# Optimization experiments

Measured on AMD Instinct MI355X. Metric: run time of the kernel, lower is better.

## Reference

```python
import jax, jax.numpy as jnp
import numpy as np

CHANNEL = 1
ALPHA = 1.0
EPS = 1e-10
SHAPE = (1, CHANNEL, 160, 192, 160)


def _sobel_kernels(channel):
    s2 = np.array([[-1., 0., 1.], [-2., 0., 2.], [-1., 0., 1.]], dtype=np.float32)
    # sobel.repeat(channel,1,3,1,1): 2D kernel tiled along depth -> k[d,h,w] = s2[h,w]
    kx = np.tile(s2[None, :, :], (3, 1, 1))
    ky = np.tile(s2.T[None, :, :], (3, 1, 1))
    kz = np.array([[[-1., -1., -1.], [-2., -2., -2.], [-1., -1., -1.]],
                   [[0., 0., 0.], [0., 0., 0.], [0., 0., 0.]],
                   [[1., 1., 1.], [2., 2., 2.], [1., 1., 1.]]], dtype=np.float32)
    def rep(k):  # -> [channel, 1, 3, 3, 3] for depthwise conv
        return jnp.asarray(np.tile(k[None, None], (channel, 1, 1, 1, 1)))
    return rep(kx), rep(ky), rep(kz)


def _conv3d(x, k, channel):
    # torch F.conv3d (cross-correlation), padding=1, groups=channel
    return jax.lax.conv_general_dilated(
        x, k, window_strides=(1, 1, 1), padding=((1, 1), (1, 1), (1, 1)),
        dimension_numbers=('NCDHW', 'OIDHW', 'NCDHW'),
        feature_group_count=channel)


def setup_inputs() -> dict:
    key = jax.random.key(0)
    k1, k2, k3 = jax.random.split(key, 3)
    M = jax.random.normal(k1, SHAPE, dtype=jnp.float32)
    S = jax.random.normal(k2, SHAPE, dtype=jnp.float32)
    flow = jax.random.normal(k3, (SHAPE[0], 3) + SHAPE[2:], dtype=jnp.float32)
    return {"M": M, "S": S, "flow": flow}


def reference(M, S, flow):
    kx, ky, kz = _sobel_kernels(CHANNEL)
    Idiff = M - S
    Sx = _conv3d(S, kx, CHANNEL)
    Sy = _conv3d(S, ky, CHANNEL)
    Sz = _conv3d(S, kz, CHANNEL)
    Mx = _conv3d(M, kx, CHANNEL)
    My = _conv3d(M, ky, CHANNEL)
    Mz = _conv3d(M, kz, CHANNEL)
    Sxyz_mag = Sx ** 2 + Sy ** 2 + Sz ** 2
    Mxyz_mag = Mx ** 2 + My ** 2 + Mz ** 2
    denom_S = Sxyz_mag + (ALPHA ** 2) * Idiff ** 2 + 1e-10
    denom_M = Mxyz_mag + (ALPHA ** 2) * Idiff ** 2 + 1e-10
    Ux = Idiff * (Sx / denom_S + Mx / denom_M)
    Uy = Idiff * (Sy / denom_S + My / denom_M)
    Uz = Idiff * (Sz / denom_S + Mz / denom_M)
    demons_ori_xz = jnp.arctan(Ux / (Uz + EPS))
    demons_ori_yz = jnp.arctan(Uy / (Uz + EPS))
    flow_ori_xz = jnp.arctan(flow[:, 0] / (flow[:, 2] + EPS))
    flow_ori_yz = jnp.arctan(flow[:, 1] / (flow[:, 2] + EPS))
    ori_error = jnp.mean((flow_ori_xz - demons_ori_xz) ** 2) + \
                jnp.mean((flow_ori_yz - demons_ori_yz) ** 2)
    return ori_error
```

## Files before the change

### kernel.cpp

```cpp
#include <hip/hip_runtime.h>
#include <math.h>

#define DD 160
#define HH 192
#define WW 160
#define TW 32
#define THB 16
#define TD 8
#define HW (HH * WW)
#define NVOX (DD * HW)
#define HTW 34
#define HTH 18
#define LSTR 34
#define HALO (HTH * HTW)

typedef float v2f __attribute__((ext_vector_type(2)));

__device__ __forceinline__ v2f vrcp(v2f a) {
    v2f r;
    r.x = __builtin_amdgcn_rcpf(a.x);
    r.y = __builtin_amdgcn_rcpf(a.y);
    return r;
}

__device__ __forceinline__ v2f atan_ratio(v2f num, v2f den) {
    v2f a = __builtin_elementwise_abs(num);
    v2f b = __builtin_elementwise_abs(den);
    v2f mn = __builtin_elementwise_min(a, b);
    v2f mx = __builtin_elementwise_max(a, b);
    v2f x = mn * vrcp(mx);
    v2f x2 = x * x;
    v2f p = __builtin_elementwise_fma(x2,
            __builtin_elementwise_fma(x2,
            __builtin_elementwise_fma(x2,
            __builtin_elementwise_fma(x2,
            __builtin_elementwise_fma(x2, (v2f)(-0.0117212f), (v2f)(0.05265332f)),
            (v2f)(-0.11643287f)), (v2f)(0.19354346f)), (v2f)(-0.33262347f)),
            (v2f)(0.99997726f));
    p *= x;
    v2f q = 1.57079632679489662f - p;
    v2f res;
    res.x = a.x > b.x ? q.x : p.x;
    res.y = a.y > b.y ? q.y : p.y;
    unsigned sx = (__float_as_uint(num.x) ^ __float_as_uint(den.x)) & 0x80000000u;
    unsigned sy = (__float_as_uint(num.y) ^ __float_as_uint(den.y)) & 0x80000000u;
    res.x = __uint_as_float(__float_as_uint(res.x) | sx);
    res.y = __uint_as_float(__float_as_uint(res.y) | sy);
    return res;
}

__global__ __launch_bounds__(256) void demons_ori_kernel(
    const float* __restrict__ Mv, const float* __restrict__ Sv,
    const float* __restrict__ flow, float* __restrict__ out)
{
    __shared__ float buf[2][2][HTH * LSTR];
    __shared__ float redbuf[4];

    const int tid = threadIdx.x;
    const int lane = tid & 63;
    const int wid = tid >> 6;
    const int i16 = lane & 15;
    const int r   = wid * 4 + (lane >> 4);
    const int tw2 = 2 * i16;
    const int w0 = blockIdx.x * TW;
    const int h0 = blockIdx.y * THB;
    const int d0 = blockIdx.z * TD;

    const bool has2 = (tid < HALO - 512);
    int gb0, gb1, gb2 = 0;
    bool ok0, ok1, ok2 = false;
    {
        int i = tid;
        int hh = i / HTW, ww = i - HTW * hh;
        int gh = h0 + hh - 1, gw = w0 + ww - 1;
        ok0 = (gh >= 0 && gh < HH && gw >= 0 && gw < WW);
        gb0 = gh * WW + gw;
        i = tid + 256;
        hh = i / HTW; ww = i - HTW * hh;
        gh = h0 + hh - 1; gw = w0 + ww - 1;
        ok1 = (gh >= 0 && gh < HH && gw >= 0 && gw < WW);
        gb1 = gh * WW + gw;
        if (has2) {
            i = tid + 512;
            hh = i / HTW; ww = i - HTW * hh;
            gh = h0 + hh - 1; gw = w0 + ww - 1;
            ok2 = (gh >= 0 && gh < HH && gw >= 0 && gw < WW);
            gb2 = gh * WW + gw;
        }
    }

    float pS0 = 0.f, pM0 = 0.f, pS1 = 0.f, pM1 = 0.f, pS2 = 0.f, pM2 = 0.f;

    auto issue = [&](int d) {
        const bool din = (d >= 0) && (d < DD);
        const size_t base = (size_t)d * HW;
        pS0 = (din && ok0) ? Sv[base + gb0] : 0.f;
        pM0 = (din && ok0) ? Mv[base + gb0] : 0.f;
        pS1 = (din && ok1) ? Sv[base + gb1] : 0.f;
        pM1 = (din && ok1) ? Mv[base + gb1] : 0.f;
        pS2 = (din && ok2) ? Sv[base + gb2] : 0.f;
        pM2 = (din && ok2) ? Mv[base + gb2] : 0.f;
    };
    auto commit = [&](int d) {
        float* __restrict__ bS = &buf[d & 1][0][0];
        float* __restrict__ bM = &buf[d & 1][1][0];
        bS[tid] = pS0;        bM[tid] = pM0;
        bS[tid + 256] = pS1;  bM[tid + 256] = pM1;
        if (has2) { bS[tid + 512] = pS2; bM[tid + 512] = pM2; }
    };

    const int rb = r * LSTR + tw2;
    auto fieldPartials = [&](const float* __restrict__ b,
                             v2f& Px, v2f& Py, v2f& Bq, v2f& Cq) {
        const float* p0 = b + rb;
        const float* p1 = p0 + LSTR;
        const float* p2 = p1 + LSTR;
        v2f lo0 = *(const v2f*)p0, hi0 = *(const v2f*)(p0 + 2);
        v2f lo1 = *(const v2f*)p1, hi1 = *(const v2f*)(p1 + 2);
        v2f lo2 = *(const v2f*)p2, hi2 = *(const v2f*)(p2 + 2);
        v2f X0 = hi0 - lo0, X1 = hi1 - lo1, X2 = hi2 - lo2;
        v2f m0 = (v2f){lo0.y, hi0.x};
        v2f m1 = (v2f){lo1.y, hi1.x};
        v2f m2 = (v2f){lo2.y, hi2.x};
        v2f s0 = lo0 + hi0, s1 = lo1 + hi1, s2 = lo2 + hi2;
        v2f W0 = __builtin_elementwise_fma(m0, (v2f)(2.f), s0);
        v2f W2 = __builtin_elementwise_fma(m2, (v2f)(2.f), s2);
        v2f I0 = s0 + m0, I1 = s1 + m1, I2 = s2 + m2;
        Px = __builtin_elementwise_fma(X1, (v2f)(2.f), X0) + X2;
        Py = W2 - W0;
        Bq = __builtin_elementwise_fma(I1, (v2f)(2.f), I0) + I2;
        Cq = m1;
    };

    v2f mSPx, mSPy, mSB, mSC, mMPx, mMPy, mMB, mMC;
    v2f zSPx, zSPy, zSB, zSC, zMPx, zMPy, zMB, zMC;
    v2f pSPx, pSPy, pSB, pSC, pMPx, pMPy, pMB, pMC;

    issue(d0 - 1);
    commit(d0 - 1);
    issue(d0);
    __syncthreads();
    fieldPartials(&buf[(d0 - 1) & 1][0][0], mSPx, mSPy, mSB, mSC);
    fieldPartials(&buf[(d0 - 1) & 1][1][0], mMPx, mMPy, mMB, mMC);
    commit(d0);
    issue(d0 + 1);
    __syncthreads();
    fieldPartials(&buf[d0 & 1][0][0], zSPx, zSPy, zSB, zSC);
    fieldPartials(&buf[d0 & 1][1][0], zMPx, zMPy, zMB, zMC);

    const size_t voffA = (size_t)(h0 + r) * WW + (w0 + tw2);
    v2f fFx, fFy, fFz;
    {
        size_t o = (size_t)d0 * HW + voffA;
        fFx = *(const v2f*)(flow + o);
        fFy = *(const v2f*)(flow + NVOX + o);
        fFz = *(const v2f*)(flow + 2 * (size_t)NVOX + o);
    }

    v2f vsum = (v2f){0.f, 0.f};

    #pragma unroll
    for (int dd = 0; dd < TD; ++dd) {
        const int d = d0 + dd;
        commit(d + 1);
        v2f nFx = (v2f){0.f, 0.f}, nFy = nFx, nFz = nFx;
        if (dd < TD - 1) {
            issue(d + 2);
            size_t o = (size_t)(d + 1) * HW + voffA;
            nFx = *(const v2f*)(flow + o);
            nFy = *(const v2f*)(flow + NVOX + o);
            nFz = *(const v2f*)(flow + 2 * (size_t)NVOX + o);
        }
        __syncthreads();
        fieldPartials(&buf[(d + 1) & 1][0][0], pSPx, pSPy, pSB, pSC);
        fieldPartials(&buf[(d + 1) & 1][1][0], pMPx, pMPy, pMB, pMC);

        v2f idf = zMC - zSC;
        v2f i2  = __builtin_elementwise_fma(idf, idf, (v2f)(1e-10f));
        v2f gxS = mSPx + zSPx + pSPx;
        v2f gyS = mSPy + zSPy + pSPy;
        v2f gzS = pSB - mSB;
        v2f gxM = mMPx + zMPx + pMPx;
        v2f gyM = mMPy + zMPy + pMPy;
        v2f gzM = pMB - mMB;
        v2f denS = __builtin_elementwise_fma(gxS, gxS,
                   __builtin_elementwise_fma(gyS, gyS,
                   __builtin_elementwise_fma(gzS, gzS, i2)));
        v2f denM = __builtin_elementwise_fma(gxM, gxM,
                   __builtin_elementwise_fma(gyM, gyM,
                   __builtin_elementwise_fma(gzM, gzM, i2)));
        v2f rS = vrcp(denS);
        v2f rM = vrcp(denM);
        v2f Ux = idf * __builtin_elementwise_fma(gxS, rS, gxM * rM);
        v2f Uy = idf * __builtin_elementwise_fma(gyS, rS, gyM * rM);
        v2f Uz = idf * __builtin_elementwise_fma(gzS, rS, gzM * rM);

        v2f uzp = Uz + 1e-10f;
        v2f dxz = atan_ratio(Ux, uzp);
        v2f dyz = atan_ratio(Uy, uzp);

        v2f fzp = fFz + 1e-10f;
        v2f fxz = atan_ratio(fFx, fzp);
        v2f fyz = atan_ratio(fFy, fzp);

        v2f e1 = fxz - dxz;
        v2f e2 = fyz - dyz;
        vsum = __builtin_elementwise_fma(e1, e1,
               __builtin_elementwise_fma(e2, e2, vsum));

        mSPx = zSPx; mSPy = zSPy; mSB = zSB; mSC = zSC;
        mMPx = zMPx; mMPy = zMPy; mMB = zMB; mMC = zMC;
        zSPx = pSPx; zSPy = pSPy; zSB = pSB; zSC = pSC;
        zMPx = pMPx; zMPy = pMPy; zMB = pMB; zMC = pMC;
        fFx = nFx; fFy = nFy; fFz = nFz;
    }

    float lsum = vsum.x + vsum.y;
    #pragma unroll
    for (int o = 32; o > 0; o >>= 1)
        lsum += __shfl_down(lsum, o, 64);
    if (lane == 0)
        redbuf[wid] = lsum;
    __syncthreads();
    if (tid == 0) {
        float s = redbuf[0] + redbuf[1] + redbuf[2] + redbuf[3];
        atomicAdd(out, s * (1.0f / (float)NVOX));
    }
}

extern "C" void kernel_launch(void* const* d_in, const int* in_sizes, int n_in,
                              void* d_out, int out_size, void* d_ws, size_t ws_size,
                              hipStream_t stream) {
    const float* Mv   = (const float*)d_in[0];
    const float* Sv   = (const float*)d_in[1];
    const float* flow = (const float*)d_in[2];
    float* out = (float*)d_out;

    hipMemsetAsync(out, 0, sizeof(float), stream);

    dim3 grid(WW / TW, HH / THB, DD / TD);
    demons_ori_kernel<<<grid, dim3(256), 0, stream>>>(Mv, Sv, flow, out);
}
```

Before: 129.5 us.

## Enlarge tile to 32x32 and compute four outputs per thread

The block tile height doubles from 16 to 32 rows, which shrinks the halo overhead per output voxel. Each thread now computes four adjacent outputs instead of two, reusing the shared LDS loads across both pairs and loading flow as float4. The cost is higher register pressure from keeping twice as many partials alive, five global loads per field per thread, and half as many blocks, which may reduce occupancy or latency hiding.

Measured after the change: 142.4 us. 1.1x slower.

```diff
diff --git a/kernel.cpp b/kernel.cpp
--- a/kernel.cpp
+++ b/kernel.cpp
@@ -5,16 +5,17 @@
 #define HH 192
 #define WW 160
 #define TW 32
-#define THB 16
+#define THB 32
 #define TD 8
 #define HW (HH * WW)
 #define NVOX (DD * HW)
 #define HTW 34
-#define HTH 18
+#define HTH 34
 #define LSTR 34
 #define HALO (HTH * HTW)
 
 typedef float v2f __attribute__((ext_vector_type(2)));
+typedef float v4f __attribute__((ext_vector_type(4)));
 
 __device__ __forceinline__ v2f vrcp(v2f a) {
     v2f r;
@@ -49,140 +50,109 @@
     return res;
 }
 
+struct Part { v2f Px, Py, B, C; };
+
 __global__ __launch_bounds__(256) void demons_ori_kernel(
     const float* __restrict__ Mv, const float* __restrict__ Sv,
     const float* __restrict__ flow, float* __restrict__ out)
 {
-    __shared__ float buf[2][2][HTH * LSTR];
+    __shared__ float buf[2][2][HALO];
     __shared__ float redbuf[4];
 
     const int tid = threadIdx.x;
     const int lane = tid & 63;
     const int wid = tid >> 6;
-    const int i16 = lane & 15;
-    const int r   = wid * 4 + (lane >> 4);
-    const int tw2 = 2 * i16;
+    const int r   = tid >> 3;
+    const int i8  = tid & 7;
+    const int tw4 = 4 * i8;
     const int w0 = blockIdx.x * TW;
     const int h0 = blockIdx.y * THB;
     const int d0 = blockIdx.z * TD;
 
-    const bool has2 = (tid < HALO - 512);
-    int gb0, gb1, gb2 = 0;
-    bool ok0, ok1, ok2 = false;
-    {
-        int i = tid;
+    const bool has4 = (tid < HALO - 1024);
+    int gb[5]; bool ok[5];
+    #pragma unroll
+    for (int s = 0; s < 5; ++s) {
+        int i = tid + 256 * s;
         int hh = i / HTW, ww = i - HTW * hh;
         int gh = h0 + hh - 1, gw = w0 + ww - 1;
-        ok0 = (gh >= 0 && gh < HH && gw >= 0 && gw < WW);
-        gb0 = gh * WW + gw;
-        i = tid + 256;
-        hh = i / HTW; ww = i - HTW * hh;
-        gh = h0 + hh - 1; gw = w0 + ww - 1;
-        ok1 = (gh >= 0 && gh < HH && gw >= 0 && gw < WW);
-        gb1 = gh * WW + gw;
-        if (has2) {
-            i = tid + 512;
-            hh = i / HTW; ww = i - HTW * hh;
-            gh = h0 + hh - 1; gw = w0 + ww - 1;
-            ok2 = (gh >= 0 && gh < HH && gw >= 0 && gw < WW);
-            gb2 = gh * WW + gw;
-        }
-    }
-
-    float pS0 = 0.f, pM0 = 0.f, pS1 = 0.f, pM1 = 0.f, pS2 = 0.f, pM2 = 0.f;
+        bool act = (s < 4) || has4;
+        ok[s] = act && (gh >= 0) && (gh < HH) && (gw >= 0) && (gw < WW);
+        gb[s] = gh * WW + gw;
+    }
+
+    float hS[5], hM[5];
 
     auto issue = [&](int d) {
-        const bool din = (d >= 0) && (d < DD);
+        const bool din = ((unsigned)d < (unsigned)DD);
         const size_t base = (size_t)d * HW;
-        pS0 = (din && ok0) ? Sv[base + gb0] : 0.f;
-        pM0 = (din && ok0) ? Mv[base + gb0] : 0.f;
-        pS1 = (din && ok1) ? Sv[base + gb1] : 0.f;
-        pM1 = (din && ok1) ? Mv[base + gb1] : 0.f;
-        pS2 = (din && ok2) ? Sv[base + gb2] : 0.f;
-        pM2 = (din && ok2) ? Mv[base + gb2] : 0.f;
+        #pragma unroll
+        for (int s = 0; s < 5; ++s) {
+            bool o = din && ok[s];
+            hS[s] = o ? Sv[base + gb[s]] : 0.f;
+            hM[s] = o ? Mv[base + gb[s]] : 0.f;
+        }
     };
     auto commit = [&](int d) {
         float* __restrict__ bS = &buf[d & 1][0][0];
         float* __restrict__ bM = &buf[d & 1][1][0];
-        bS[tid] = pS0;        bM[tid] = pM0;
-        bS[tid + 256] = pS1;  bM[tid + 256] = pM1;
-        if (has2) { bS[tid + 512] = pS2; bM[tid + 512] = pM2; }
-    };
-
-    const int rb = r * LSTR + tw2;
-    auto fieldPartials = [&](const float* __restrict__ b,
-                             v2f& Px, v2f& Py, v2f& Bq, v2f& Cq) {
+        #pragma unroll
+        for (int s = 0; s < 4; ++s) {
+            bS[tid + 256 * s] = hS[s];
+            bM[tid + 256 * s] = hM[s];
+        }
+        if (has4) { bS[tid + 1024] = hS[4]; bM[tid + 1024] = hM[4]; }
+    };
+
+    const int rb = r * LSTR + tw4;
+    auto fieldPartials = [&](const float* __restrict__ b, Part& A, Part& B) {
         const float* p0 = b + rb;
         const float* p1 = p0 + LSTR;
         const float* p2 = p1 + LSTR;
-        v2f lo0 = *(const v2f*)p0, hi0 = *(const v2f*)(p0 + 2);
-        v2f lo1 = *(const v2f*)p1, hi1 = *(const v2f*)(p1 + 2);
-        v2f lo2 = *(const v2f*)p2, hi2 = *(const v2f*)(p2 + 2);
-        v2f X0 = hi0 - lo0, X1 = hi1 - lo1, X2 = hi2 - lo2;
-        v2f m0 = (v2f){lo0.y, hi0.x};
-        v2f m1 = (v2f){lo1.y, hi1.x};
-        v2f m2 = (v2f){lo2.y, hi2.x};
-        v2f s0 = lo0 + hi0, s1 = lo1 + hi1, s2 = lo2 + hi2;
-        v2f W0 = __builtin_elementwise_fma(m0, (v2f)(2.f), s0);
-        v2f W2 = __builtin_elementwise_fma(m2, (v2f)(2.f), s2);
-        v2f I0 = s0 + m0, I1 = s1 + m1, I2 = s2 + m2;
-        Px = __builtin_elementwise_fma(X1, (v2f)(2.f), X0) + X2;
-        Py = W2 - W0;
-        Bq = __builtin_elementwise_fma(I1, (v2f)(2.f), I0) + I2;
-        Cq = m1;
-    };
-
-    v2f mSPx, mSPy, mSB, mSC, mMPx, mMPy, mMB, mMC;
-    v2f zSPx, zSPy, zSB, zSC, zMPx, zMPy, zMB, zMC;
-    v2f pSPx, pSPy, pSB, pSC, pMPx, pMPy, pMB, pMC;
-
-    issue(d0 - 1);
-    commit(d0 - 1);
-    issue(d0);
-    __syncthreads();
-    fieldPartials(&buf[(d0 - 1) & 1][0][0], mSPx, mSPy, mSB, mSC);
-    fieldPartials(&buf[(d0 - 1) & 1][1][0], mMPx, mMPy, mMB, mMC);
-    commit(d0);
-    issue(d0 + 1);
-    __syncthreads();
-    fieldPartials(&buf[d0 & 1][0][0], zSPx, zSPy, zSB, zSC);
-    fieldPartials(&buf[d0 & 1][1][0], zMPx, zMPy, zMB, zMC);
-
-    const size_t voffA = (size_t)(h0 + r) * WW + (w0 + tw2);
-    v2f fFx, fFy, fFz;
-    {
-        size_t o = (size_t)d0 * HW + voffA;
-        fFx = *(const v2f*)(flow + o);
-        fFy = *(const v2f*)(flow + NVOX + o);
-        fFz = *(const v2f*)(flow + 2 * (size_t)NVOX + o);
-    }
-
-    v2f vsum = (v2f){0.f, 0.f};
-
-    #pragma unroll
-    for (int dd = 0; dd < TD; ++dd) {
-        const int d = d0 + dd;
-        commit(d + 1);
-        v2f nFx = (v2f){0.f, 0.f}, nFy = nFx, nFz = nFx;
-        if (dd < TD - 1) {
-            issue(d + 2);
-            size_t o = (size_t)(d + 1) * HW + voffA;
-            nFx = *(const v2f*)(flow + o);
-            nFy = *(const v2f*)(flow + NVOX + o);
-            nFz = *(const v2f*)(flow + 2 * (size_t)NVOX + o);
-        }
-        __syncthreads();
-        fieldPartials(&buf[(d + 1) & 1][0][0], pSPx, pSPy, pSB, pSC);
-        fieldPartials(&buf[(d + 1) & 1][1][0], pMPx, pMPy, pMB, pMC);
-
-        v2f idf = zMC - zSC;
+        v2f a0 = *(const v2f*)p0, b0 = *(const v2f*)(p0 + 2), c0 = *(const v2f*)(p0 + 4);
+        v2f a1 = *(const v2f*)p1, b1 = *(const v2f*)(p1 + 2), c1 = *(const v2f*)(p1 + 4);
+        v2f a2 = *(const v2f*)p2, b2 = *(const v2f*)(p2 + 2), c2 = *(const v2f*)(p2 + 4);
+        {
+            v2f X0 = b0 - a0, X1 = b1 - a1, X2 = b2 - a2;
+            v2f m0 = (v2f){a0.y, b0.x};
+            v2f m1 = (v2f){a1.y, b1.x};
+            v2f m2 = (v2f){a2.y, b2.x};
+            v2f s0 = a0 + b0, s1 = a1 + b1, s2 = a2 + b2;
+            v2f W0 = __builtin_elementwise_fma(m0, (v2f)(2.f), s0);
+            v2f W2 = __builtin_elementwise_fma(m2, (v2f)(2.f), s2);
+            v2f I0 = s0 + m0, I1 = s1 + m1, I2 = s2 + m2;
+            A.Px = __builtin_elementwise_fma(X1, (v2f)(2.f), X0) + X2;
+            A.Py = W2 - W0;
+            A.B  = __builtin_elementwise_fma(I1, (v2f)(2.f), I0) + I2;
+            A.C  = m1;
+        }
+        {
+            v2f X0 = c0 - b0, X1 = c1 - b1, X2 = c2 - b2;
+            v2f m0 = (v2f){b0.y, c0.x};
+            v2f m1 = (v2f){b1.y, c1.x};
+            v2f m2 = (v2f){b2.y, c2.x};
+            v2f s0 = b0 + c0, s1 = b1 + c1, s2 = b2 + c2;
+            v2f W0 = __builtin_elementwise_fma(m0, (v2f)(2.f), s0);
+            v2f W2 = __builtin_elementwise_fma(m2, (v2f)(2.f), s2);
+            v2f I0 = s0 + m0, I1 = s1 + m1, I2 = s2 + m2;
+            B.Px = __builtin_elementwise_fma(X1, (v2f)(2.f), X0) + X2;
+            B.Py = W2 - W0;
+            B.B  = __builtin_elementwise_fma(I1, (v2f)(2.f), I0) + I2;
+            B.C  = m1;
+        }
+    };
+
+    auto pairTerm = [&](const Part& mSk, const Part& zSk, const Part& pSk,
+                        const Part& mMk, const Part& zMk, const Part& pMk,
+                        v2f fx, v2f fy, v2f fz) -> v2f {
+        v2f idf = zMk.C - zSk.C;
         v2f i2  = __builtin_elementwise_fma(idf, idf, (v2f)(1e-10f));
-        v2f gxS = mSPx + zSPx + pSPx;
-        v2f gyS = mSPy + zSPy + pSPy;
-        v2f gzS = pSB - mSB;
-        v2f gxM = mMPx + zMPx + pMPx;
-        v2f gyM = mMPy + zMPy + pMPy;
-        v2f gzM = pMB - mMB;
+        v2f gxS = mSk.Px + zSk.Px + pSk.Px;
+        v2f gyS = mSk.Py + zSk.Py + pSk.Py;
+        v2f gzS = pSk.B - mSk.B;
+        v2f gxM = mMk.Px + zMk.Px + pMk.Px;
+        v2f gyM = mMk.Py + zMk.Py + pMk.Py;
+        v2f gzM = pMk.B - mMk.B;
         v2f denS = __builtin_elementwise_fma(gxS, gxS,
                    __builtin_elementwise_fma(gyS, gyS,
                    __builtin_elementwise_fma(gzS, gzS, i2)));
@@ -194,24 +164,68 @@
         v2f Ux = idf * __builtin_elementwise_fma(gxS, rS, gxM * rM);
         v2f Uy = idf * __builtin_elementwise_fma(gyS, rS, gyM * rM);
         v2f Uz = idf * __builtin_elementwise_fma(gzS, rS, gzM * rM);
-
         v2f uzp = Uz + 1e-10f;
         v2f dxz = atan_ratio(Ux, uzp);
         v2f dyz = atan_ratio(Uy, uzp);
-
-        v2f fzp = fFz + 1e-10f;
-        v2f fxz = atan_ratio(fFx, fzp);
-        v2f fyz = atan_ratio(fFy, fzp);
-
+        v2f fzp = fz + 1e-10f;
+        v2f fxz = atan_ratio(fx, fzp);
+        v2f fyz = atan_ratio(fy, fzp);
         v2f e1 = fxz - dxz;
         v2f e2 = fyz - dyz;
-        vsum = __builtin_elementwise_fma(e1, e1,
-               __builtin_elementwise_fma(e2, e2, vsum));
-
-        mSPx = zSPx; mSPy = zSPy; mSB = zSB; mSC = zSC;
-        mMPx = zMPx; mMPy = zMPy; mMB = zMB; mMC = zMC;
-        zSPx = pSPx; zSPy = pSPy; zSB = pSB; zSC = pSC;
-        zMPx = pMPx; zMPy = pMPy; zMB = pMB; zMC = pMC;
+        return __builtin_elementwise_fma(e1, e1, e2 * e2);
+    };
+
+    Part mS[2], zS[2], pP[2], mM[2], zM[2], pQ[2];
+
+    issue(d0 - 1);
+    commit(d0 - 1);
+    issue(d0);
+    __syncthreads();
+    fieldPartials(&buf[(d0 - 1) & 1][0][0], mS[0], mS[1]);
+    fieldPartials(&buf[(d0 - 1) & 1][1][0], mM[0], mM[1]);
+    commit(d0);
+    issue(d0 + 1);
+    __syncthreads();
+    fieldPartials(&buf[d0 & 1][0][0], zS[0], zS[1]);
+    fieldPartials(&buf[d0 & 1][1][0], zM[0], zM[1]);
+
+    const size_t voffA = (size_t)(h0 + r) * WW + (w0 + tw4);
+    v4f fFx, fFy, fFz;
+    {
+        size_t o = (size_t)d0 * HW + voffA;
+        fFx = *(const v4f*)(flow + o);
+        fFy = *(const v4f*)(flow + NVOX + o);
+        fFz = *(const v4f*)(flow + 2 * (size_t)NVOX + o);
+    }
+
+    v2f vsum = (v2f){0.f, 0.f};
+
+    #pragma unroll
+    for (int dd = 0; dd < TD; ++dd) {
+        const int d = d0 + dd;
+        commit(d + 1);
+        v4f nFx = (v4f){0.f, 0.f, 0.f, 0.f}, nFy = nFx, nFz = nFx;
+        if (dd < TD - 1) {
+            issue(d + 2);
+            size_t o = (size_t)(d + 1) * HW + voffA;
+            nFx = *(const v4f*)(flow + o);
+            nFy = *(const v4f*)(flow + NVOX + o);
+            nFz = *(const v4f*)(flow + 2 * (size_t)NVOX + o);
+        }
+        __syncthreads();
+        fieldPartials(&buf[(d + 1) & 1][0][0], pP[0], pP[1]);
+        fieldPartials(&buf[(d + 1) & 1][1][0], pQ[0], pQ[1]);
+
+        vsum += pairTerm(mS[0], zS[0], pP[0], mM[0], zM[0], pQ[0],
+                         (v2f){fFx.x, fFx.y}, (v2f){fFy.x, fFy.y}, (v2f){fFz.x, fFz.y});
+        vsum += pairTerm(mS[1], zS[1], pP[1], mM[1], zM[1], pQ[1],
+                         (v2f){fFx.z, fFx.w}, (v2f){fFy.z, fFy.w}, (v2f){fFz.z, fFz.w});
+
+        #pragma unroll
+        for (int k = 0; k < 2; ++k) {
+            mS[k] = zS[k]; zS[k] = pP[k];
+            mM[k] = zM[k]; zM[k] = pQ[k];
+        }
         fFx = nFx; fFy = nFy; fFz = nFz;
     }
 
```

## Replace LDS halo staging with direct global vector loads per thread

Applied to the files above, without the earlier changes.

Removes the shared-memory double-buffered halo tile and the per-plane __syncthreads. Each thread now loads its 3x3 neighbourhood rows directly from global memory as float2 vectors (left, center, right) and relies on the L1/L2 caches for reuse between neighbours. This avoids LDS writes, reads and block barriers, at the cost of about nine redundant global loads per plane per field and no explicit software prefetch of the next plane.

Measured after the change: 203.3 us. +57.0%, slower.

```diff
diff --git a/kernel.cpp b/kernel.cpp
--- a/kernel.cpp
+++ b/kernel.cpp
@@ -9,10 +9,6 @@
 #define TD 8
 #define HW (HH * WW)
 #define NVOX (DD * HW)
-#define HTW 34
-#define HTH 18
-#define LSTR 34
-#define HALO (HTH * HTW)
 
 typedef float v2f __attribute__((ext_vector_type(2)));
 
@@ -49,109 +45,87 @@
     return res;
 }
 
+struct Part { v2f Px, Py, B, C; };
+
 __global__ __launch_bounds__(256) void demons_ori_kernel(
     const float* __restrict__ Mv, const float* __restrict__ Sv,
     const float* __restrict__ flow, float* __restrict__ out)
 {
-    __shared__ float buf[2][2][HTH * LSTR];
     __shared__ float redbuf[4];
 
     const int tid = threadIdx.x;
     const int lane = tid & 63;
     const int wid = tid >> 6;
-    const int i16 = lane & 15;
-    const int r   = wid * 4 + (lane >> 4);
-    const int tw2 = 2 * i16;
-    const int w0 = blockIdx.x * TW;
-    const int h0 = blockIdx.y * THB;
-    const int d0 = blockIdx.z * TD;
-
-    const bool has2 = (tid < HALO - 512);
-    int gb0, gb1, gb2 = 0;
-    bool ok0, ok1, ok2 = false;
-    {
-        int i = tid;
-        int hh = i / HTW, ww = i - HTW * hh;
-        int gh = h0 + hh - 1, gw = w0 + ww - 1;
-        ok0 = (gh >= 0 && gh < HH && gw >= 0 && gw < WW);
-        gb0 = gh * WW + gw;
-        i = tid + 256;
-        hh = i / HTW; ww = i - HTW * hh;
-        gh = h0 + hh - 1; gw = w0 + ww - 1;
-        ok1 = (gh >= 0 && gh < HH && gw >= 0 && gw < WW);
-        gb1 = gh * WW + gw;
-        if (has2) {
-            i = tid + 512;
-            hh = i / HTW; ww = i - HTW * hh;
-            gh = h0 + hh - 1; gw = w0 + ww - 1;
-            ok2 = (gh >= 0 && gh < HH && gw >= 0 && gw < WW);
-            gb2 = gh * WW + gw;
-        }
-    }
-
-    float pS0 = 0.f, pM0 = 0.f, pS1 = 0.f, pM1 = 0.f, pS2 = 0.f, pM2 = 0.f;
-
-    auto issue = [&](int d) {
-        const bool din = (d >= 0) && (d < DD);
-        const size_t base = (size_t)d * HW;
-        pS0 = (din && ok0) ? Sv[base + gb0] : 0.f;
-        pM0 = (din && ok0) ? Mv[base + gb0] : 0.f;
-        pS1 = (din && ok1) ? Sv[base + gb1] : 0.f;
-        pM1 = (din && ok1) ? Mv[base + gb1] : 0.f;
-        pS2 = (din && ok2) ? Sv[base + gb2] : 0.f;
-        pM2 = (din && ok2) ? Mv[base + gb2] : 0.f;
+    const int i16 = tid & 15;
+    const int r   = tid >> 4;
+    const int gw  = blockIdx.x * TW + 2 * i16;
+    const int gh  = blockIdx.y * THB + r;
+    const int d0  = blockIdx.z * TD;
+
+    const bool okL = (gw >= 2);
+    const bool okR = (gw + 3 < WW);
+    const bool okU = (gh >= 1);
+    const bool okD = (gh + 1 < HH);
+
+    auto planeField = [&](const float* __restrict__ f, int d, Part& P) {
+        const bool din = ((unsigned)d < (unsigned)DD);
+        const float* pc = f + (long)d * HW + (long)gh * WW + gw;
+        v2f zero = (v2f)(0.f);
+        v2f X0, X1, X2, W0, W2, I0, I1, I2, Cmid;
+        {
+            const float* p = pc - WW;
+            bool rok = din && okU;
+            v2f L = (rok && okL) ? *(const v2f*)(p - 2) : zero;
+            v2f C = rok ? *(const v2f*)p : zero;
+            v2f R = (rok && okR) ? *(const v2f*)(p + 2) : zero;
+            v2f cA = (v2f){L.y, C.x};
+            v2f cC = (v2f){C.y, R.x};
+            v2f s = cA + cC;
+            X0 = cC - cA;
+            W0 = __builtin_elementwise_fma(C, (v2f)(2.f), s);
+            I0 = s + C;
+        }
+        {
+            const float* p = pc;
+            v2f L = (din && okL) ? *(const v2f*)(p - 2) : zero;
+            v2f C = din ? *(const v2f*)p : zero;
+            v2f R = (din && okR) ? *(const v2f*)(p + 2) : zero;
+            v2f cA = (v2f){L.y, C.x};
+            v2f cC = (v2f){C.y, R.x};
+            v2f s = cA + cC;
+            X1 = cC - cA;
+            I1 = s + C;
+            Cmid = C;
+        }
+        {
+            const float* p = pc + WW;
+            bool rok = din && okD;
+            v2f L = (rok && okL) ? *(const v2f*)(p - 2) : zero;
+            v2f C = rok ? *(const v2f*)p : zero;
+            v2f R = (rok && okR) ? *(const v2f*)(p + 2) : zero;
+            v2f cA = (v2f){L.y, C.x};
+            v2f cC = (v2f){C.y, R.x};
+            v2f s = cA + cC;
+            X2 = cC - cA;
+            W2 = __builtin_elementwise_fma(C, (v2f)(2.f), s);
+            I2 = s + C;
+        }
+        P.Px = __builtin_elementwise_fma(X1, (v2f)(2.f), X0) + X2;
+        P.Py = W2 - W0;
+        P.B  = __builtin_elementwise_fma(I1, (v2f)(2.f), I0) + I2;
+        P.C  = Cmid;
     };
-    auto commit = [&](int d) {
-        float* __restrict__ bS = &buf[d & 1][0][0];
-        float* __restrict__ bM = &buf[d & 1][1][0];
-        bS[tid] = pS0;        bM[tid] = pM0;
-        bS[tid + 256] = pS1;  bM[tid + 256] = pM1;
-        if (has2) { bS[tid + 512] = pS2; bM[tid + 512] = pM2; }
-    };
-
-    const int rb = r * LSTR + tw2;
-    auto fieldPartials = [&](const float* __restrict__ b,
-                             v2f& Px, v2f& Py, v2f& Bq, v2f& Cq) {
-        const float* p0 = b + rb;
-        const float* p1 = p0 + LSTR;
-        const float* p2 = p1 + LSTR;
-        v2f lo0 = *(const v2f*)p0, hi0 = *(const v2f*)(p0 + 2);
-        v2f lo1 = *(const v2f*)p1, hi1 = *(const v2f*)(p1 + 2);
-        v2f lo2 = *(const v2f*)p2, hi2 = *(const v2f*)(p2 + 2);
-        v2f X0 = hi0 - lo0, X1 = hi1 - lo1, X2 = hi2 - lo2;
-        v2f m0 = (v2f){lo0.y, hi0.x};
-        v2f m1 = (v2f){lo1.y, hi1.x};
-        v2f m2 = (v2f){lo2.y, hi2.x};
-        v2f s0 = lo0 + hi0, s1 = lo1 + hi1, s2 = lo2 + hi2;
-        v2f W0 = __builtin_elementwise_fma(m0, (v2f)(2.f), s0);
-        v2f W2 = __builtin_elementwise_fma(m2, (v2f)(2.f), s2);
-        v2f I0 = s0 + m0, I1 = s1 + m1, I2 = s2 + m2;
-        Px = __builtin_elementwise_fma(X1, (v2f)(2.f), X0) + X2;
-        Py = W2 - W0;
-        Bq = __builtin_elementwise_fma(I1, (v2f)(2.f), I0) + I2;
-        Cq = m1;
-    };
-
-    v2f mSPx, mSPy, mSB, mSC, mMPx, mMPy, mMB, mMC;
-    v2f zSPx, zSPy, zSB, zSC, zMPx, zMPy, zMB, zMC;
-    v2f pSPx, pSPy, pSB, pSC, pMPx, pMPy, pMB, pMC;
-
-    issue(d0 - 1);
-    commit(d0 - 1);
-    issue(d0);
-    __syncthreads();
-    fieldPartials(&buf[(d0 - 1) & 1][0][0], mSPx, mSPy, mSB, mSC);
-    fieldPartials(&buf[(d0 - 1) & 1][1][0], mMPx, mMPy, mMB, mMC);
-    commit(d0);
-    issue(d0 + 1);
-    __syncthreads();
-    fieldPartials(&buf[d0 & 1][0][0], zSPx, zSPy, zSB, zSC);
-    fieldPartials(&buf[d0 & 1][1][0], zMPx, zMPy, zMB, zMC);
-
-    const size_t voffA = (size_t)(h0 + r) * WW + (w0 + tw2);
+
+    Part mS, zS, pS, mM, zM, pM;
+    planeField(Sv, d0 - 1, mS);
+    planeField(Mv, d0 - 1, mM);
+    planeField(Sv, d0, zS);
+    planeField(Mv, d0, zM);
+
+    const size_t voff = (size_t)gh * WW + gw;
     v2f fFx, fFy, fFz;
     {
-        size_t o = (size_t)d0 * HW + voffA;
+        size_t o = (size_t)d0 * HW + voff;
         fFx = *(const v2f*)(flow + o);
         fFy = *(const v2f*)(flow + NVOX + o);
         fFz = *(const v2f*)(flow + 2 * (size_t)NVOX + o);
@@ -162,27 +136,24 @@
     #pragma unroll
     for (int dd = 0; dd < TD; ++dd) {
         const int d = d0 + dd;
-        commit(d + 1);
+        planeField(Sv, d + 1, pS);
+        planeField(Mv, d + 1, pM);
         v2f nFx = (v2f){0.f, 0.f}, nFy = nFx, nFz = nFx;
         if (dd < TD - 1) {
-            issue(d + 2);
-            size_t o = (size_t)(d + 1) * HW + voffA;
+            size_t o = (size_t)(d + 1) * HW + voff;
             nFx = *(const v2f*)(flow + o);
             nFy = *(const v2f*)(flow + NVOX + o);
             nFz = *(const v2f*)(flow + 2 * (size_t)NVOX + o);
         }
-        __syncthreads();
-        fieldPartials(&buf[(d + 1) & 1][0][0], pSPx, pSPy, pSB, pSC);
-        fieldPartials(&buf[(d + 1) & 1][1][0], pMPx, pMPy, pMB, pMC);
-
-        v2f idf = zMC - zSC;
+
+        v2f idf = zM.C - zS.C;
         v2f i2  = __builtin_elementwise_fma(idf, idf, (v2f)(1e-10f));
-        v2f gxS = mSPx + zSPx + pSPx;
-        v2f gyS = mSPy + zSPy + pSPy;
-        v2f gzS = pSB - mSB;
-        v2f gxM = mMPx + zMPx + pMPx;
-        v2f gyM = mMPy + zMPy + pMPy;
-        v2f gzM = pMB - mMB;
+        v2f gxS = mS.Px + zS.Px + pS.Px;
+        v2f gyS = mS.Py + zS.Py + pS.Py;
+        v2f gzS = pS.B - mS.B;
+        v2f gxM = mM.Px + zM.Px + pM.Px;
+        v2f gyM = mM.Py + zM.Py + pM.Py;
+        v2f gzM = pM.B - mM.B;
         v2f denS = __builtin_elementwise_fma(gxS, gxS,
                    __builtin_elementwise_fma(gyS, gyS,
                    __builtin_elementwise_fma(gzS, gzS, i2)));
@@ -208,10 +179,8 @@
         vsum = __builtin_elementwise_fma(e1, e1,
                __builtin_elementwise_fma(e2, e2, vsum));
 
-        mSPx = zSPx; mSPy = zSPy; mSB = zSB; mSC = zSC;
-        mMPx = zMPx; mMPy = zMPy; mMB = zMB; mMC = zMC;
-        zSPx = pSPx; zSPy = pSPy; zSB = pSB; zSC = pSC;
-        zMPx = pMPx; zMPy = pMPy; zMB = pMB; zMC = pMC;
+        mS = zS; zS = pS;
+        mM = zM; zM = pM;
         fFx = nFx; fFy = nFy; fFz = nFz;
     }
 
```
